# Kernel tuning notes

Hardware: AMD Instinct MI355X
Metric: run time of the kernel (lower is better)

Reference implementation:

```python
import jax, jax.numpy as jnp
import numpy as np

EMBED_DIM = 1024
NUM_HEADS = 16
HEAD_DIM = EMBED_DIM // NUM_HEADS


def setup_inputs() -> dict:
    key = jax.random.key(0)
    ks = jax.random.split(key, 6)
    B, S, D = 4, 2048, EMBED_DIM
    scale = 1.0 / np.sqrt(D)
    x = jax.random.normal(ks[0], (B, S, D), dtype=jnp.float32)
    mask = jnp.ones((B, S), dtype=jnp.int32)
    Wq = jax.random.normal(ks[1], (D, D), dtype=jnp.float32) * scale
    Wk = jax.random.normal(ks[2], (D, D), dtype=jnp.float32) * scale
    Wv = jax.random.normal(ks[3], (D, D), dtype=jnp.float32) * scale
    Wo = jax.random.normal(ks[4], (D, D), dtype=jnp.float32) * scale
    bq = jnp.zeros((D,), jnp.float32)
    bk = jnp.zeros((D,), jnp.float32)
    bv = jnp.zeros((D,), jnp.float32)
    bo = jnp.zeros((D,), jnp.float32)
    return {"x": x, "mask": mask, "Wq": Wq, "bq": bq, "Wk": Wk, "bk": bk,
            "Wv": Wv, "bv": bv, "Wo": Wo, "bo": bo}


def reference(x, mask, Wq, bq, Wk, bk, Wv, bv, Wo, bo):
    B, S, D = x.shape
    H, Hd = NUM_HEADS, HEAD_DIM

    def split_heads(t):  # [B,S,D] -> [B,H,S,Hd]
        return t.reshape(B, S, H, Hd).transpose(0, 2, 1, 3)

    q = split_heads(x @ Wq.T + bq)
    k = split_heads(x @ Wk.T + bk)
    v = split_heads(x @ Wv.T + bv)

    scores = jnp.einsum('bhqd,bhkd->bhqk', q, k) / jnp.sqrt(jnp.float32(Hd))
    # mask [B,S] -> broadcast over heads and query positions: [B,1,1,S]
    m = mask[:, None, None, :]
    scores = jnp.where(m == 0, jnp.float32(-1e9), scores)
    attn = jax.nn.softmax(scores, axis=-1)  # dropout_rate=0.0 (eval)
    out = jnp.einsum('bhqk,bhkd->bhqd', attn, v)
    out = out.transpose(0, 2, 1, 3).reshape(B, S, D)
    return out @ Wo.T + bo
```

## Files before the change

### kernel.cpp

```cpp
#include <hip/hip_runtime.h>
#include <stdint.h>

typedef __attribute__((ext_vector_type(8))) short short8;
typedef __attribute__((ext_vector_type(4))) float floatx4;
typedef __attribute__((ext_vector_type(16))) float f32x16;
typedef __attribute__((ext_vector_type(4))) unsigned int uint4v;

#define D_MODEL 1024
#define SEQ     2048
#define NHEAD   16
#define HDIM    64
#define BATCH   4
#define NW      (D_MODEL * D_MODEL)

__device__ __forceinline__ unsigned short f2b(float f) {
  unsigned int u = __builtin_bit_cast(unsigned int, f);
  u += 0x7FFFu + ((u >> 16) & 1u);
  return (unsigned short)(u >> 16);
}

__device__ __forceinline__ floatx4 mfma16(short8 a, short8 b, floatx4 c) {
  return __builtin_amdgcn_mfma_f32_16x16x32_bf16(a, b, c, 0, 0, 0);
}
__device__ __forceinline__ f32x16 mfma32(short8 a, short8 b, f32x16 c) {
  return __builtin_amdgcn_mfma_f32_32x32x16_bf16(a, b, c, 0, 0, 0);
}
__device__ __forceinline__ unsigned int cvtpk(float lo, float hi) {
  unsigned int r;
  asm("v_cvt_pk_bf16_f32 %0, %1, %2" : "=v"(r) : "v"(lo), "v"(hi));
  return r;
}
__device__ __forceinline__ void pl32swap(unsigned int &a, unsigned int &b) {
  asm("v_permlane32_swap_b32 %0, %1" : "+v"(a), "+v"(b));
}
__device__ __forceinline__ float expfast(float x) {
  return __builtin_amdgcn_exp2f(x);
}

#define GLL16(gsrc, ldst)                                                     \
  __builtin_amdgcn_global_load_lds(                                           \
      (const __attribute__((address_space(1))) void*)(gsrc),                  \
      (__attribute__((address_space(3))) void*)(ldst), 16, 0, 0)

__global__ void cvt_f32_bf16(const float* __restrict__ in,
                             unsigned short* __restrict__ out, int n) {
  int idx = (blockIdx.x * blockDim.x + threadIdx.x) * 4;
  int stride = gridDim.x * blockDim.x * 4;
  for (int i = idx; i < n; i += stride) {
    float4 v = *reinterpret_cast<const float4*>(in + i);
    ushort4 o;
    o.x = f2b(v.x); o.y = f2b(v.y); o.z = f2b(v.z); o.w = f2b(v.w);
    *reinterpret_cast<ushort4*>(out + i) = o;
  }
}

__global__ void cvt_w(const float* __restrict__ Wq, const float* __restrict__ Wk,
                      const float* __restrict__ Wv, const float* __restrict__ Wo,
                      unsigned short* __restrict__ Wqkv,
                      unsigned short* __restrict__ Wob,
                      const int* __restrict__ mask, float* __restrict__ maskb) {
  const int which = blockIdx.y;
  int idx = (blockIdx.x * blockDim.x + threadIdx.x) * 4;
  int stride = gridDim.x * blockDim.x * 4;
  if (which == 4) {
    for (int i = idx; i < BATCH * SEQ; i += stride) {
      int4 mv = *reinterpret_cast<const int4*>(mask + i);
      float4 o;
      o.x = mv.x ? 0.f : -1e10f;
      o.y = mv.y ? 0.f : -1e10f;
      o.z = mv.z ? 0.f : -1e10f;
      o.w = mv.w ? 0.f : -1e10f;
      *reinterpret_cast<float4*>(maskb + i) = o;
    }
    return;
  }
  const float* s = which == 0 ? Wq : which == 1 ? Wk : which == 2 ? Wv : Wo;
  unsigned short* d = which < 3 ? Wqkv + (size_t)which * NW : Wob;
  for (int i = idx; i < NW; i += stride) {
    float4 v = *reinterpret_cast<const float4*>(s + i);
    ushort4 o;
    o.x = f2b(v.x); o.y = f2b(v.y); o.z = f2b(v.z); o.w = f2b(v.w);
    *reinterpret_cast<ushort4*>(d + i) = o;
  }
}

__global__ void mask_flags(const int* __restrict__ mask,
                           unsigned int* __restrict__ flags2,
                           const float* __restrict__ bq,
                           const float* __restrict__ bk,
                           const float* __restrict__ bv,
                           float* __restrict__ bqkv) {
  const int b = blockIdx.x, tid = threadIdx.x;
  if (tid < 64) {
    int ok = 0;
    if (tid < 32) {
      ok = 1;
      for (int i = 0; i < 64; ++i) ok &= mask[b * SEQ + tid * 64 + i];
    }
    unsigned long long bal = __ballot(ok);
    if (tid == 0) flags2[b] = (unsigned int)bal;
  }
  const int i = blockIdx.x * 256 + tid;
  bqkv[i] = bq[i];
  bqkv[1024 + i] = bk[i];
  bqkv[2048 + i] = bv[i];
}

template <int MODE>
__global__ __launch_bounds__(256) void gemm_bt(
    const unsigned short* __restrict__ A, const unsigned short* __restrict__ B,
    const float* __restrict__ bias, void* __restrict__ C,
    unsigned short* __restrict__ VT, int M, int N, int K) {
  __shared__ __align__(16) unsigned short As[128 * 64];
  __shared__ __align__(16) unsigned short Bs[128 * 64];
  const int tid = threadIdx.x;
  const int w = tid >> 6, l = tid & 63, lg = l >> 4, li = l & 15;
  const int GX = (MODE == 1) ? 24 : 8;
  const int NWG = GX * 64;
  int id = blockIdx.y * GX + blockIdx.x;
  id = (id & 7) * (NWG >> 3) + (id >> 3);
  const int m0 = (id / GX) * 128, n0 = (id % GX) * 128;
  const int wr = w >> 1, wc = w & 1;

  floatx4 acc[4][4];
#pragma unroll
  for (int m = 0; m < 4; ++m)
#pragma unroll
    for (int n = 0; n < 4; ++n) acc[m][n] = (floatx4){0.f, 0.f, 0.f, 0.f};

  for (int k0 = 0; k0 < K; k0 += 64) {
    __syncthreads();
#pragma unroll
    for (int p = 0; p < 4; ++p) {
      const int c = p * 256 + tid;
      const int row = c >> 3;
      const int co = (c & 7) * 8;
      GLL16(A + (size_t)(m0 + row) * K + k0 + co, As + (p * 256 + w * 64) * 8);
      GLL16(B + (size_t)(n0 + row) * K + k0 + co, Bs + (p * 256 + w * 64) * 8);
    }
    __syncthreads();
#pragma unroll
    for (int kk = 0; kk < 2; ++kk) {
      short8 af[4], bfr[4];
#pragma unroll
      for (int m = 0; m < 4; ++m)
        af[m] = *reinterpret_cast<const short8*>(
            &As[(wr * 64 + m * 16 + li) * 64 + kk * 32 + lg * 8]);
#pragma unroll
      for (int n = 0; n < 4; ++n)
        bfr[n] = *reinterpret_cast<const short8*>(
            &Bs[(wc * 64 + n * 16 + li) * 64 + kk * 32 + lg * 8]);
#pragma unroll
      for (int m = 0; m < 4; ++m)
#pragma unroll
        for (int n = 0; n < 4; ++n) acc[m][n] = mfma16(af[m], bfr[n], acc[m][n]);
    }
  }

#pragma unroll
  for (int m = 0; m < 4; ++m)
#pragma unroll
    for (int n = 0; n < 4; ++n) {
      const int gcol = n0 + wc * 64 + n * 16 + li;
      const float bv = bias[gcol];
      const int grow0 = m0 + wr * 64 + m * 16 + lg * 4;
      if (MODE == 1 && n0 >= 2048) {
        const int vc = gcol - 2048;
        const int hh = vc >> 6, dd = vc & 63;
        const int b = grow0 >> 11, s0 = grow0 & 2047;
        ushort4 pk;
        pk.x = f2b(acc[m][n][0] + bv);
        pk.y = f2b(acc[m][n][1] + bv);
        pk.z = f2b(acc[m][n][2] + bv);
        pk.w = f2b(acc[m][n][3] + bv);
        *reinterpret_cast<ushort4*>(
            &VT[((size_t)((b * NHEAD + hh) * HDIM + dd)) * SEQ + s0]) = pk;
      } else {
        const float scl =
            (MODE == 1 && gcol < 1024) ? 0.18033688011112042f : 1.f;
#pragma unroll
        for (int r = 0; r < 4; ++r) {
          const float val = (acc[m][n][r] + bv) * scl;
          if (MODE == 2)
            reinterpret_cast<float*>(C)[(size_t)(grow0 + r) * N + gcol] = val;
          else
            reinterpret_cast<unsigned short*>(C)[(size_t)(grow0 + r) * N + gcol] =
                f2b(val);
        }
      }
    }
}

__global__ __launch_bounds__(512) void attn_v7(
    const unsigned short* __restrict__ QKV, const unsigned short* __restrict__ VT,
    const float* __restrict__ maskb, const unsigned int* __restrict__ flags2,
    unsigned short* __restrict__ O) {
  __shared__ __align__(16) unsigned short Kl[2][64 * 64];
  __shared__ __align__(16) unsigned short Vl[2][64 * 64];
  const int tid = threadIdx.x, w = tid >> 6, l = tid & 63;
  const int qi = l & 31, hi = l >> 5;
  const int bid = blockIdx.x;
  const int qblk = bid >> 6, bh = bid & 63, b = bh >> 4, h = bh & 15;
  const int q0 = qblk * 256 + w * 32;

  const unsigned short* qptr = QKV + (size_t)(b * SEQ + q0 + qi) * 3072 + h * 64;
  short8 qf[4];
#pragma unroll
  for (int ds = 0; ds < 4; ++ds)
    qf[ds] = *reinterpret_cast<const short8*>(qptr + ds * 16 + hi * 8);

  int off[2][4];
#pragma unroll
  for (int kb = 0; kb < 2; ++kb)
#pragma unroll
    for (int ds = 0; ds < 4; ++ds)
      off[kb][ds] = (kb * 32 + qi) * 64 + (((ds * 2 + hi) ^ (qi & 7)) * 8);

  const int srow = tid >> 3;
  const int swz = ((tid & 7) ^ (srow & 7)) * 8;
  const int ldst = w * 512;
  const unsigned short* kp0 =
      QKV + (size_t)(b * SEQ) * 3072 + D_MODEL + h * 64 + (size_t)srow * 3072 + swz;
  const unsigned short* vp0 =
      VT + (size_t)((b * NHEAD + h) * HDIM) * SEQ + (size_t)srow * SEQ + swz;

#define STAGE(BUF)                                                             \
  do {                                                                         \
    GLL16(kp0, &Kl[BUF][ldst]);                                                \
    GLL16(vp0, &Vl[BUF][ldst]);                                                \
    kp0 += 64 * 3072; vp0 += 64;                                               \
  } while (0)

  const float* mrow = maskb + b * SEQ;
  const unsigned int fl = flags2[b];
  f32x16 oa[2] = {};
  float l_run = 0.f;

#define TILE(BUF, KT)                                                          \
  do {                                                                         \
    f32x16 pa0 = {}, pa1 = {};                                                 \
    __builtin_amdgcn_s_setprio(1);                                             \
    _Pragma("unroll") for (int ds = 0; ds < 4; ++ds) {                         \
      const short8 kf0 =                                                       \
          *reinterpret_cast<const short8*>(&Kl[BUF][off[0][ds]]);              \
      const short8 kf1 =                                                       \
          *reinterpret_cast<const short8*>(&Kl[BUF][off[1][ds]]);              \
      pa0 = mfma32(kf0, qf[ds], pa0);                                          \
      pa1 = mfma32(kf1, qf[ds], pa1);                                          \
    }                                                                          \
    __builtin_amdgcn_s_setprio(0);                                             \
    if (!((fl >> (KT)) & 1)) {                \
      _Pragma("unroll") for (int rq = 0; rq < 4; ++rq) {                       \
        const float4 m0 = *reinterpret_cast<const float4*>(                    \
            mrow + (KT) * 64 + rq * 8 + hi * 4);                               \
        const float4 m1 = *reinterpret_cast<const float4*>(                    \
            mrow + (KT) * 64 + 32 + rq * 8 + hi * 4);                          \
        pa0[rq * 4 + 0] += m0.x; pa0[rq * 4 + 1] += m0.y;                      \
        pa0[rq * 4 + 2] += m0.z; pa0[rq * 4 + 3] += m0.w;                      \
        pa1[rq * 4 + 0] += m1.x; pa1[rq * 4 + 1] += m1.y;                      \
        pa1[rq * 4 + 2] += m1.z; pa1[rq * 4 + 3] += m1.w;                      \
      }                                                                        \
    }                                                                          \
    float r0 = 0.f, r1 = 0.f, r2 = 0.f, r3 = 0.f;                              \
    _Pragma("unroll") for (int r = 0; r < 16; r += 4) {                        \
      float p;                                                                 \
      p = expfast(pa0[r + 0]); pa0[r + 0] = p; r0 += p;                        \
      p = expfast(pa0[r + 1]); pa0[r + 1] = p; r1 += p;                        \
      p = expfast(pa0[r + 2]); pa0[r + 2] = p; r2 += p;                        \
      p = expfast(pa0[r + 3]); pa0[r + 3] = p; r3 += p;                        \
      p = expfast(pa1[r + 0]); pa1[r + 0] = p; r0 += p;                        \
      p = expfast(pa1[r + 1]); pa1[r + 1] = p; r1 += p;                        \
      p = expfast(pa1[r + 2]); pa1[r + 2] = p; r2 += p;                        \
      p = expfast(pa1[r + 3]); pa1[r + 3] = p; r3 += p;                        \
    }                                                                          \
    l_run += (r0 + r1) + (r2 + r3);                                            \
    unsigned int c0[8], c1[8];                                                 \
    _Pragma("unroll") for (int u2 = 0; u2 < 8; ++u2) {                         \
      c0[u2] = cvtpk(pa0[2 * u2], pa0[2 * u2 + 1]);                            \
      c1[u2] = cvtpk(pa1[2 * u2], pa1[2 * u2 + 1]);                            \
    }                                                                          \
    pl32swap(c0[0], c0[2]); pl32swap(c0[1], c0[3]);                            \
    pl32swap(c0[4], c0[6]); pl32swap(c0[5], c0[7]);                            \
    pl32swap(c1[0], c1[2]); pl32swap(c1[1], c1[3]);                            \
    pl32swap(c1[4], c1[6]); pl32swap(c1[5], c1[7]);                            \
    __builtin_amdgcn_s_setprio(1);                                             \
    _Pragma("unroll") for (int ks = 0; ks < 4; ++ks) {                         \
      const int kb = ks >> 1, hf = (ks & 1) * 4;                               \
      const short8 pf = __builtin_bit_cast(                                    \
          short8, kb ? (uint4v){c1[hf], c1[hf + 1], c1[hf + 2], c1[hf + 3]}    \
                     : (uint4v){c0[hf], c0[hf + 1], c0[hf + 2], c0[hf + 3]});  \
      const short8 vf0 =                                                       \
          *reinterpret_cast<const short8*>(&Vl[BUF][off[0][ks]]);              \
      const short8 vf1 =                                                       \
          *reinterpret_cast<const short8*>(&Vl[BUF][off[1][ks]]);              \
      oa[0] = mfma32(vf0, pf, oa[0]);                                          \
      oa[1] = mfma32(vf1, pf, oa[1]);                                          \
    }                                                                          \
    __builtin_amdgcn_s_setprio(0);                                             \
  } while (0)

  STAGE(0);
  __syncthreads();
#pragma unroll 1
  for (int kt = 0; kt < 32; kt += 2) {
    STAGE(1);
    TILE(0, kt);
    __syncthreads();
    if (kt + 2 < 32) STAGE(0);
    TILE(1, kt + 1);
    __syncthreads();
  }
#undef STAGE
#undef TILE

  l_run += __shfl_xor(l_run, 32);
  const float rinv = 1.f / l_run;
  unsigned int u[2][8];
#pragma unroll
  for (int vb = 0; vb < 2; ++vb) {
#pragma unroll
    for (int uu = 0; uu < 8; ++uu)
      u[vb][uu] = cvtpk(oa[vb][2 * uu] * rinv, oa[vb][2 * uu + 1] * rinv);
    pl32swap(u[vb][0], u[vb][2]);
    pl32swap(u[vb][1], u[vb][3]);
    pl32swap(u[vb][4], u[vb][6]);
    pl32swap(u[vb][5], u[vb][7]);
  }
  unsigned short* optr = O + (size_t)(b * SEQ + q0 + qi) * D_MODEL + h * 64;
#pragma unroll
  for (int cix = 0; cix < 4; ++cix) {
    const int vb = cix >> 1, hf = (cix & 1) * 4;
    *reinterpret_cast<short8*>(optr + cix * 16 + hi * 8) = __builtin_bit_cast(
        short8,
        (uint4v){u[vb][hf], u[vb][hf + 1], u[vb][hf + 2], u[vb][hf + 3]});
  }
}

extern "C" void kernel_launch(void* const* d_in, const int* in_sizes, int n_in,
                              void* d_out, int out_size, void* d_ws, size_t ws_size,
                              hipStream_t stream) {
  const float* x  = (const float*)d_in[0];
  const int* mask = (const int*)d_in[1];
  const float* Wq = (const float*)d_in[2];
  const float* bq = (const float*)d_in[3];
  const float* Wk = (const float*)d_in[4];
  const float* bk = (const float*)d_in[5];
  const float* Wv = (const float*)d_in[6];
  const float* bv = (const float*)d_in[7];
  const float* Wo = (const float*)d_in[8];
  const float* bo = (const float*)d_in[9];

  char* ws = (char*)d_ws;
  const size_t SZ_X = (size_t)BATCH * SEQ * D_MODEL * 2;
  unsigned short* xb    = (unsigned short*)(ws);
  unsigned short* Wqkvb = (unsigned short*)(ws + SZ_X);
  unsigned short* Wob   = (unsigned short*)(ws + SZ_X + 6u * 1024 * 1024);
  unsigned short* QKVb  = (unsigned short*)(ws + 24u * 1024 * 1024);
  unsigned short* VTb   = (unsigned short*)(ws + 72u * 1024 * 1024);
  float*          bqkv  = (float*)(ws + 88u * 1024 * 1024);
  float*          maskb = (float*)(ws + 88u * 1024 * 1024 + 16384);
  unsigned int*   flag2 = (unsigned int*)(ws + 88u * 1024 * 1024 + 49152);
  unsigned short* Ob    = xb;

  const int NX = BATCH * SEQ * D_MODEL;
  const int M = BATCH * SEQ;

  cvt_f32_bf16<<<2048, 256, 0, stream>>>(x, xb, NX);
  cvt_w<<<dim3(512, 5), 256, 0, stream>>>(Wq, Wk, Wv, Wo, Wqkvb, Wob, mask, maskb);
  mask_flags<<<BATCH, 256, 0, stream>>>(mask, flag2, bq, bk, bv, bqkv);

  gemm_bt<1><<<dim3(3 * D_MODEL / 128, M / 128), 256, 0, stream>>>(
      xb, Wqkvb, bqkv, QKVb, VTb, M, 3 * D_MODEL, D_MODEL);

  attn_v7<<<BATCH * NHEAD * (SEQ / 256), 512, 0, stream>>>(QKVb, VTb, maskb,
                                                           flag2, Ob);

  gemm_bt<2><<<dim3(D_MODEL / 128, M / 128), 256, 0, stream>>>(
      Ob, Wob, bo, d_out, nullptr, M, D_MODEL, D_MODEL);
}
```

Before: 213.6 us.

## Double-buffer GEMM LDS tiles with XOR swizzle and MFMA priority boost

The projection GEMM now keeps two LDS buffers for A and B. It issues the global-to-LDS loads for the next K tile while the current tile runs through MFMA, so there is one barrier per tile instead of two. The 16-byte chunk index is XOR-swizzled by row on load and on read to reduce LDS bank conflicts, and s_setprio raises wave priority around the MFMA block. The cost is twice the LDS per block, which may lower occupancy, and the loop assumes an even number of K tiles.

```diff
diff --git a/kernel.cpp b/kernel.cpp
--- a/kernel.cpp
+++ b/kernel.cpp
@@ -111,8 +111,8 @@
     const unsigned short* __restrict__ A, const unsigned short* __restrict__ B,
     const float* __restrict__ bias, void* __restrict__ C,
     unsigned short* __restrict__ VT, int M, int N, int K) {
-  __shared__ __align__(16) unsigned short As[128 * 64];
-  __shared__ __align__(16) unsigned short Bs[128 * 64];
+  __shared__ __align__(16) unsigned short As[2][128 * 64];
+  __shared__ __align__(16) unsigned short Bs[2][128 * 64];
   const int tid = threadIdx.x;
   const int w = tid >> 6, l = tid & 63, lg = l >> 4, li = l & 15;
   const int GX = (MODE == 1) ? 24 : 8;
@@ -128,34 +128,53 @@
 #pragma unroll
     for (int n = 0; n < 4; ++n) acc[m][n] = (floatx4){0.f, 0.f, 0.f, 0.f};
 
-  for (int k0 = 0; k0 < K; k0 += 64) {
+#define GSTAGE(BUF, T)                                                         \
+  do {                                                                         \
+    _Pragma("unroll") for (int p = 0; p < 4; ++p) {                            \
+      const int c = p * 256 + tid;                                             \
+      const int row = c >> 3;                                                  \
+      const int co = ((c & 7) ^ (row & 7)) * 8;                                \
+      GLL16(A + (size_t)(m0 + row) * K + (T) * 64 + co,                        \
+            &As[BUF][(p * 256 + w * 64) * 8]);                                 \
+      GLL16(B + (size_t)(n0 + row) * K + (T) * 64 + co,                        \
+            &Bs[BUF][(p * 256 + w * 64) * 8]);                                 \
+    }                                                                          \
+  } while (0)
+
+#define GCOMP(BUF)                                                             \
+  do {                                                                         \
+    _Pragma("unroll") for (int kk = 0; kk < 2; ++kk) {                         \
+      short8 af[4], bfr[4];                                                    \
+      _Pragma("unroll") for (int m = 0; m < 4; ++m)                            \
+        af[m] = *reinterpret_cast<const short8*>(                              \
+            &As[BUF][(wr * 64 + m * 16 + li) * 64 +                            \
+                     (((kk * 4 + lg) ^ (li & 7)) * 8)]);                       \
+      _Pragma("unroll") for (int n = 0; n < 4; ++n)                            \
+        bfr[n] = *reinterpret_cast<const short8*>(                             \
+            &Bs[BUF][(wc * 64 + n * 16 + li) * 64 +                            \
+                     (((kk * 4 + lg) ^ (li & 7)) * 8)]);                       \
+      __builtin_amdgcn_s_setprio(1);                                           \
+      _Pragma("unroll") for (int m = 0; m < 4; ++m)                            \
+        _Pragma("unroll") for (int n = 0; n < 4; ++n)                          \
+            acc[m][n] = mfma16(af[m], bfr[n], acc[m][n]);                      \
+      __builtin_amdgcn_s_setprio(0);                                           \
+    }                                                                          \
+  } while (0)
+
+  const int NT = K >> 6;
+  GSTAGE(0, 0);
+  __syncthreads();
+#pragma unroll 1
+  for (int t = 0; t < NT; t += 2) {
+    if (t + 1 < NT) GSTAGE(1, t + 1);
+    GCOMP(0);
     __syncthreads();
-#pragma unroll
-    for (int p = 0; p < 4; ++p) {
-      const int c = p * 256 + tid;
-      const int row = c >> 3;
-      const int co = (c & 7) * 8;
-      GLL16(A + (size_t)(m0 + row) * K + k0 + co, As + (p * 256 + w * 64) * 8);
-      GLL16(B + (size_t)(n0 + row) * K + k0 + co, Bs + (p * 256 + w * 64) * 8);
-    }
+    if (t + 2 < NT) GSTAGE(0, t + 2);
+    GCOMP(1);
     __syncthreads();
-#pragma unroll
-    for (int kk = 0; kk < 2; ++kk) {
-      short8 af[4], bfr[4];
-#pragma unroll
-      for (int m = 0; m < 4; ++m)
-        af[m] = *reinterpret_cast<const short8*>(
-            &As[(wr * 64 + m * 16 + li) * 64 + kk * 32 + lg * 8]);
-#pragma unroll
-      for (int n = 0; n < 4; ++n)
-        bfr[n] = *reinterpret_cast<const short8*>(
-            &Bs[(wc * 64 + n * 16 + li) * 64 + kk * 32 + lg * 8]);
-#pragma unroll
-      for (int m = 0; m < 4; ++m)
-#pragma unroll
-        for (int n = 0; n < 4; ++n) acc[m][n] = mfma16(af[m], bfr[n], acc[m][n]);
-    }
-  }
+  }
+#undef GSTAGE
+#undef GCOMP
 
 #pragma unroll
   for (int m = 0; m < 4; ++m)
```

After: 185.5 us. -13.2%, faster.

## Rewrite projection GEMM as 8-wave 256x128 tile with triple-buffered LDS pipeline

Applied to the files above, without the earlier changes.

Replaces the 4-wave 128x128 GEMM with an 8-wave 256x128 block that triple-buffers A/B tiles in LDS, prefetching two K-tiles ahead and interleaving global-to-LDS loads with MFMA phases. It also adds an XOR swizzle on LDS columns to avoid bank conflicts, and raises MFMA priority with setprio. The goal is to hide global load latency and barrier stalls behind MFMA work. In exchange it uses much more LDS (144 KB per block), which limits occupancy, and it hardcodes K=1024 (16 tiles) in the loop schedule.

```diff
diff --git a/kernel.cpp b/kernel.cpp
--- a/kernel.cpp
+++ b/kernel.cpp
@@ -107,19 +107,19 @@
 }
 
 template <int MODE>
-__global__ __launch_bounds__(256) void gemm_bt(
+__global__ __launch_bounds__(512) void gemm8(
     const unsigned short* __restrict__ A, const unsigned short* __restrict__ B,
     const float* __restrict__ bias, void* __restrict__ C,
     unsigned short* __restrict__ VT, int M, int N, int K) {
-  __shared__ __align__(16) unsigned short As[128 * 64];
-  __shared__ __align__(16) unsigned short Bs[128 * 64];
+  __shared__ __align__(16) unsigned short As[3][256 * 64];
+  __shared__ __align__(16) unsigned short Bs[3][128 * 64];
   const int tid = threadIdx.x;
   const int w = tid >> 6, l = tid & 63, lg = l >> 4, li = l & 15;
   const int GX = (MODE == 1) ? 24 : 8;
-  const int NWG = GX * 64;
+  const int NWG = GX * (M >> 8);
   int id = blockIdx.y * GX + blockIdx.x;
   id = (id & 7) * (NWG >> 3) + (id >> 3);
-  const int m0 = (id / GX) * 128, n0 = (id % GX) * 128;
+  const int m0 = (id / GX) * 256, n0 = (id % GX) * 128;
   const int wr = w >> 1, wc = w & 1;
 
   floatx4 acc[4][4];
@@ -128,34 +128,104 @@
 #pragma unroll
     for (int n = 0; n < 4; ++n) acc[m][n] = (floatx4){0.f, 0.f, 0.f, 0.f};
 
-  for (int k0 = 0; k0 < K; k0 += 64) {
-    __syncthreads();
-#pragma unroll
-    for (int p = 0; p < 4; ++p) {
-      const int c = p * 256 + tid;
-      const int row = c >> 3;
-      const int co = (c & 7) * 8;
-      GLL16(A + (size_t)(m0 + row) * K + k0 + co, As + (p * 256 + w * 64) * 8);
-      GLL16(B + (size_t)(n0 + row) * K + k0 + co, Bs + (p * 256 + w * 64) * 8);
-    }
-    __syncthreads();
-#pragma unroll
-    for (int kk = 0; kk < 2; ++kk) {
-      short8 af[4], bfr[4];
-#pragma unroll
-      for (int m = 0; m < 4; ++m)
-        af[m] = *reinterpret_cast<const short8*>(
-            &As[(wr * 64 + m * 16 + li) * 64 + kk * 32 + lg * 8]);
-#pragma unroll
-      for (int n = 0; n < 4; ++n)
-        bfr[n] = *reinterpret_cast<const short8*>(
-            &Bs[(wc * 64 + n * 16 + li) * 64 + kk * 32 + lg * 8]);
-#pragma unroll
-      for (int m = 0; m < 4; ++m)
-#pragma unroll
-        for (int n = 0; n < 4; ++n) acc[m][n] = mfma16(af[m], bfr[n], acc[m][n]);
-    }
-  }
+#define STA(BUF, T, P)                                                         \
+  do {                                                                         \
+    const int c_ = (P) * 512 + tid;                                            \
+    const int row_ = c_ >> 3;                                                  \
+    const int co_ = ((c_ & 7) ^ (row_ & 7)) * 8;                               \
+    GLL16(A + (size_t)(m0 + row_) * K + (T) * 64 + co_,                        \
+          &As[BUF][((P) * 512 + w * 64) * 8]);                                 \
+  } while (0)
+#define STB(BUF, T, P)                                                         \
+  do {                                                                         \
+    const int c_ = (P) * 512 + tid;                                            \
+    const int row_ = c_ >> 3;                                                  \
+    const int co_ = ((c_ & 7) ^ (row_ & 7)) * 8;                               \
+    GLL16(B + (size_t)(n0 + row_) * K + (T) * 64 + co_,                        \
+          &Bs[BUF][((P) * 512 + w * 64) * 8]);                                 \
+  } while (0)
+#define STAGE6(BUF, T)                                                         \
+  do {                                                                         \
+    STA(BUF, T, 0); STA(BUF, T, 1); STA(BUF, T, 2); STA(BUF, T, 3);            \
+    STB(BUF, T, 0); STB(BUF, T, 1);                                            \
+  } while (0)
+
+#define RA(BUF, MM, KK)                                                        \
+  (*reinterpret_cast<const short8*>(                                           \
+      &As[BUF][(wr * 64 + (MM) * 16 + li) * 64 + (((KK)*4 + lg) ^ (li & 7)) * 8]))
+#define RB(BUF, NN, KK)                                                        \
+  (*reinterpret_cast<const short8*>(                                           \
+      &Bs[BUF][(wc * 64 + (NN) * 16 + li) * 64 + (((KK)*4 + lg) ^ (li & 7)) * 8]))
+
+#define PHASE_SYNC()                                                           \
+  do {                                                                         \
+    __builtin_amdgcn_s_barrier();                                              \
+    asm volatile("s_waitcnt lgkmcnt(0)" ::: "memory");                         \
+    __builtin_amdgcn_sched_barrier(0);                                         \
+  } while (0)
+
+#define MFMA8(AF0, AF1, M0, M1)                                                \
+  do {                                                                         \
+    __builtin_amdgcn_s_setprio(1);                                             \
+    acc[M0][0] = mfma16(AF0, bf0, acc[M0][0]);                                 \
+    acc[M0][1] = mfma16(AF0, bf1, acc[M0][1]);                                 \
+    acc[M0][2] = mfma16(AF0, bf2, acc[M0][2]);                                 \
+    acc[M0][3] = mfma16(AF0, bf3, acc[M0][3]);                                 \
+    acc[M1][0] = mfma16(AF1, bf0, acc[M1][0]);                                 \
+    acc[M1][1] = mfma16(AF1, bf1, acc[M1][1]);                                 \
+    acc[M1][2] = mfma16(AF1, bf2, acc[M1][2]);                                 \
+    acc[M1][3] = mfma16(AF1, bf3, acc[M1][3]);                                 \
+    __builtin_amdgcn_s_setprio(0);                                             \
+  } while (0)
+
+#define KTILE(BUF, SB, T, VMC, DOST)                                           \
+  do {                                                                         \
+    asm volatile("s_waitcnt vmcnt(" #VMC ")" ::: "memory");                    \
+    __builtin_amdgcn_s_barrier();                                              \
+    __builtin_amdgcn_sched_barrier(0);                                         \
+                                                     \
+    short8 af0 = RA(BUF, 0, 0), af1 = RA(BUF, 1, 0);                           \
+    short8 bf0 = RB(BUF, 0, 0), bf1 = RB(BUF, 1, 0);                           \
+    short8 bf2 = RB(BUF, 2, 0), bf3 = RB(BUF, 3, 0);                           \
+    if (DOST) { STA(SB, (T) + 2, 0); STA(SB, (T) + 2, 1); }                    \
+    PHASE_SYNC();                                                              \
+    MFMA8(af0, af1, 0, 1);                                                     \
+                                                     \
+    short8 af2 = RA(BUF, 2, 0), af3 = RA(BUF, 3, 0);                           \
+    if (DOST) { STA(SB, (T) + 2, 2); STA(SB, (T) + 2, 3); }                    \
+    PHASE_SYNC();                                                              \
+    MFMA8(af2, af3, 2, 3);                                                     \
+                                                     \
+    af0 = RA(BUF, 0, 1); af1 = RA(BUF, 1, 1);                                  \
+    bf0 = RB(BUF, 0, 1); bf1 = RB(BUF, 1, 1);                                  \
+    bf2 = RB(BUF, 2, 1); bf3 = RB(BUF, 3, 1);                                  \
+    if (DOST) { STB(SB, (T) + 2, 0); }                                         \
+    PHASE_SYNC();                                                              \
+    MFMA8(af0, af1, 0, 1);                                                     \
+                                                     \
+    af2 = RA(BUF, 2, 1); af3 = RA(BUF, 3, 1);                                  \
+    if (DOST) { STB(SB, (T) + 2, 1); }                                         \
+    PHASE_SYNC();                                                              \
+    MFMA8(af2, af3, 2, 3);                                                     \
+  } while (0)
+
+  STAGE6(0, 0);
+  STAGE6(1, 1);
+#pragma unroll 1
+  for (int t = 0; t < 15; t += 3) {
+    KTILE(0, 2, t, 6, true);
+    KTILE(1, 0, t + 1, 6, true);
+    KTILE(2, 1, t + 2, 6, (t + 4) < 16);
+  }
+  KTILE(0, 0, 15, 0, false);
+#undef STA
+#undef STB
+#undef STAGE6
+#undef RA
+#undef RB
+#undef PHASE_SYNC
+#undef MFMA8
+#undef KTILE
 
 #pragma unroll
   for (int m = 0; m < 4; ++m)
@@ -369,12 +439,12 @@
   cvt_w<<<dim3(512, 5), 256, 0, stream>>>(Wq, Wk, Wv, Wo, Wqkvb, Wob, mask, maskb);
   mask_flags<<<BATCH, 256, 0, stream>>>(mask, flag2, bq, bk, bv, bqkv);
 
-  gemm_bt<1><<<dim3(3 * D_MODEL / 128, M / 128), 256, 0, stream>>>(
+  gemm8<1><<<dim3(3 * D_MODEL / 128, M / 256), 512, 0, stream>>>(
       xb, Wqkvb, bqkv, QKVb, VTb, M, 3 * D_MODEL, D_MODEL);
 
   attn_v7<<<BATCH * NHEAD * (SEQ / 256), 512, 0, stream>>>(QKVb, VTb, maskb,
                                                            flag2, Ob);
 
-  gemm_bt<2><<<dim3(D_MODEL / 128, M / 128), 256, 0, stream>>>(
+  gemm8<2><<<dim3(D_MODEL / 128, M / 256), 512, 0, stream>>>(
       Ob, Wob, bo, d_out, nullptr, M, D_MODEL, D_MODEL);
 }
```

Result: faster. 191.9 us (-10.2%).
